# Performance work log

Hardware: AMD Instinct MI355X
Metric: run time of the kernel (lower is better)

Reference implementation:

```python
import jax, jax.numpy as jnp
import numpy as np

N_NODES = 25000
N_EDGES = 400000
D = 128            # input_dim == all gnn_latent_dim entries
N_LAYERS = 3
N_GRAPHS = 512
D_OUT = 10
BN_EPS = 1e-5


def setup_inputs() -> dict:
    key = jax.random.key(0)
    ks = jax.random.split(key, 12)
    s = 1.0 / np.sqrt(D)
    x = jax.random.normal(ks[0], (N_NODES, D), dtype=jnp.float32)
    edge_index = jax.random.randint(ks[1], (2, N_EDGES), 0, N_NODES, dtype=jnp.int64)
    batch = jnp.sort(jax.random.randint(ks[2], (N_NODES,), 0, N_GRAPHS, dtype=jnp.int64))
    W1 = jax.random.normal(ks[3], (N_LAYERS, D, D), dtype=jnp.float32) * s
    b1 = jnp.zeros((N_LAYERS, D), dtype=jnp.float32)
    gamma = jnp.ones((N_LAYERS, D), dtype=jnp.float32)
    beta = jnp.zeros((N_LAYERS, D), dtype=jnp.float32)
    run_mean = jnp.zeros((N_LAYERS, D), dtype=jnp.float32)
    run_var = jnp.ones((N_LAYERS, D), dtype=jnp.float32)
    W2 = jax.random.normal(ks[4], (N_LAYERS, D, D), dtype=jnp.float32) * s
    b2 = jnp.zeros((N_LAYERS, D), dtype=jnp.float32)
    eps = jnp.zeros((N_LAYERS,), dtype=jnp.float32)  # GIN eps, train_eps=True init 0
    Wout = jax.random.normal(ks[5], (D, D_OUT), dtype=jnp.float32) * s
    bout = jnp.zeros((D_OUT,), dtype=jnp.float32)
    return {"x": x, "edge_index": edge_index, "batch": batch,
            "W1": W1, "b1": b1, "gamma": gamma, "beta": beta,
            "run_mean": run_mean, "run_var": run_var,
            "W2": W2, "b2": b2, "eps": eps, "Wout": Wout, "bout": bout}


def reference(x, edge_index, batch, W1, b1, gamma, beta, run_mean, run_var, W2, b2, eps, Wout, bout):
    src, dst = edge_index[0], edge_index[1]
    h = x
    for i in range(N_LAYERS):
        # GIN aggregation: sum_{j in N(i)} h_j + (1 + eps) * h_i  (self loop weight 1+eps)
        agg = jax.ops.segment_sum(h[src], dst, num_segments=N_NODES)
        agg = agg + (1.0 + eps[i]) * h
        # nn: Linear -> BatchNorm1d (eval, running stats) -> ReLU -> Linear
        z = agg @ W1[i] + b1[i]
        z = (z - run_mean[i]) * jax.lax.rsqrt(run_var[i] + BN_EPS) * gamma[i] + beta[i]
        z = jax.nn.relu(z)
        z = z @ W2[i] + b2[i]
        # post-conv activation (dropout p=0 omitted)
        h = jax.nn.relu(z)
    # readout: global mean pool per graph
    ones = jnp.ones((h.shape[0],), dtype=h.dtype)
    counts = jax.ops.segment_sum(ones, batch, num_segments=N_GRAPHS)
    pooled = jax.ops.segment_sum(h, batch, num_segments=N_GRAPHS) / jnp.clip(counts, 1.0)[:, None]
    # single final Linear (fc_latent_dim=[])
    logits = pooled @ Wout + bout
    return logits
```

## Files before the change

kernel.cpp:

```cpp
#include <hip/hip_runtime.h>
#include <hip/hip_bf16.h>

#define NNODES 25000
#define NEDGES 400000
#define DIM 128
#define NGRAPHS 512
#define DOUT 10
#define NPAD 32768

typedef short bf16x8 __attribute__((ext_vector_type(8)));
typedef float f32x4 __attribute__((ext_vector_type(4)));

__device__ inline float bfu_lo(unsigned int u) {
  union { unsigned int i; float f; } v; v.i = u << 16; return v.f;
}
__device__ inline float bfu_hi(unsigned int u) {
  union { unsigned int i; float f; } v; v.i = u & 0xffff0000u; return v.f;
}
__device__ inline unsigned short f2bf(float f) {
  union { float f; unsigned int i; } v; v.f = f;
  unsigned int r = v.i + 0x7fff + ((v.i >> 16) & 1);
  return (unsigned short)(r >> 16);
}


__global__ __launch_bounds__(256) void k_deg(const int* __restrict__ dst,
                                             int* __restrict__ deg) {
  int i = blockIdx.x * 256 + threadIdx.x;
  if (i < NEDGES) atomicAdd(&deg[dst[i]], 1);
}

__global__ __launch_bounds__(1024) void k_scan(const int* __restrict__ deg,
                                               int* __restrict__ offs,
                                               int* __restrict__ cursor) {
  __shared__ int tsum[1024];
  int t = threadIdx.x;
  const int4* d4 = (const int4*)(deg + t * 32);
  int4 v[8];
#pragma unroll
  for (int j = 0; j < 8; ++j) v[j] = d4[j];
  int s = 0;
#pragma unroll
  for (int j = 0; j < 8; ++j) s += v[j].x + v[j].y + v[j].z + v[j].w;
  tsum[t] = s;
  __syncthreads();
  for (int off = 1; off < 1024; off <<= 1) {
    int u = (t >= off) ? tsum[t - off] : 0;
    __syncthreads();
    tsum[t] += u;
    __syncthreads();
  }
  int run = (t == 0) ? 0 : tsum[t - 1];
  int4* o4 = (int4*)(offs + t * 32);
  int4* c4 = (int4*)(cursor + t * 32);
#pragma unroll
  for (int j = 0; j < 8; ++j) {
    int4 w;
    w.x = run; run += v[j].x;
    w.y = run; run += v[j].y;
    w.z = run; run += v[j].z;
    w.w = run; run += v[j].w;
    o4[j] = w; c4[j] = w;
  }
}

__global__ __launch_bounds__(256) void k_scatter(const int* __restrict__ src,
                                                 const int* __restrict__ dst,
                                                 int* __restrict__ cursor,
                                                 int* __restrict__ csr) {
  int i = blockIdx.x * 256 + threadIdx.x;
  if (i < NEDGES) {
    int p = atomicAdd(&cursor[dst[i]], 1);
    csr[p] = src[i];
  }
}


__global__ __launch_bounds__(256) void k_cvt(const float* __restrict__ x,
                                             unsigned short* __restrict__ h0) {
  int i = blockIdx.x * 256 + threadIdx.x;
  if (i * 8 >= NNODES * DIM) return;
  const float4* x4 = (const float4*)x;
  float4 a = x4[i * 2], b = x4[i * 2 + 1];
  uint4 p;
  p.x = ((unsigned int)f2bf(a.y) << 16) | f2bf(a.x);
  p.y = ((unsigned int)f2bf(a.w) << 16) | f2bf(a.z);
  p.z = ((unsigned int)f2bf(b.y) << 16) | f2bf(b.x);
  p.w = ((unsigned int)f2bf(b.w) << 16) | f2bf(b.z);
  ((uint4*)h0)[i] = p;
}


__global__ __launch_bounds__(256) void k_wprep(const float* __restrict__ W1,
                                               const float* __restrict__ W2,
                                               unsigned short* __restrict__ W1T,
                                               unsigned short* __restrict__ W2T) {
  int b = blockIdx.x;
  int l = b >> 1;
  const float* in = ((b & 1) ? W2 : W1) + (size_t)l * DIM * DIM;
  unsigned short* out = ((b & 1) ? W2T : W1T) + (size_t)l * DIM * DIM;
  for (int idx = threadIdx.x; idx < DIM * DIM; idx += 256) {
    int c = idx >> 7, k = idx & 127;
    out[idx] = f2bf(in[k * DIM + c]);
  }
}


__global__ __launch_bounds__(256) void k_agg(const unsigned short* __restrict__ h,
                                             const int* __restrict__ offs,
                                             const int* __restrict__ csr,
                                             const float* __restrict__ epsp, int layer,
                                             unsigned short* __restrict__ agg) {
  int node = blockIdx.x * 8 + (threadIdx.x >> 5);
  int lane = threadIdx.x & 31;
  const uint2* h2 = (const uint2*)h;
  float eps1 = 1.0f + epsp[layer];
  int s = offs[node], e = offs[node + 1];
  uint2 hv = h2[(size_t)node * 32 + lane];
  float a0 = eps1 * bfu_lo(hv.x), a1 = eps1 * bfu_hi(hv.x);
  float a2 = eps1 * bfu_lo(hv.y), a3 = eps1 * bfu_hi(hv.y);
  float b0 = 0.f, b1 = 0.f, b2 = 0.f, b3 = 0.f;
  int j = s;
  for (; j + 3 < e; j += 4) {
    int s0 = csr[j], s1 = csr[j + 1], s2 = csr[j + 2], s3 = csr[j + 3];
    uint2 v0 = h2[(size_t)s0 * 32 + lane];
    uint2 v1 = h2[(size_t)s1 * 32 + lane];
    uint2 v2 = h2[(size_t)s2 * 32 + lane];
    uint2 v3 = h2[(size_t)s3 * 32 + lane];
    a0 += bfu_lo(v0.x); a1 += bfu_hi(v0.x); a2 += bfu_lo(v0.y); a3 += bfu_hi(v0.y);
    b0 += bfu_lo(v1.x); b1 += bfu_hi(v1.x); b2 += bfu_lo(v1.y); b3 += bfu_hi(v1.y);
    a0 += bfu_lo(v2.x); a1 += bfu_hi(v2.x); a2 += bfu_lo(v2.y); a3 += bfu_hi(v2.y);
    b0 += bfu_lo(v3.x); b1 += bfu_hi(v3.x); b2 += bfu_lo(v3.y); b3 += bfu_hi(v3.y);
  }
  for (; j < e; ++j) {
    uint2 v = h2[(size_t)csr[j] * 32 + lane];
    a0 += bfu_lo(v.x); a1 += bfu_hi(v.x); a2 += bfu_lo(v.y); a3 += bfu_hi(v.y);
  }
  a0 += b0; a1 += b1; a2 += b2; a3 += b3;
  uint2 p;
  p.x = ((unsigned int)f2bf(a1) << 16) | f2bf(a0);
  p.y = ((unsigned int)f2bf(a3) << 16) | f2bf(a2);
  ((uint2*)agg)[(size_t)node * 32 + lane] = p;
}


#define MROWS 32

__global__ __launch_bounds__(256) void k_mlp(const unsigned short* __restrict__ agg,
                                             const unsigned short* __restrict__ W1T,
                                             const unsigned short* __restrict__ W2T,
                                             const float* __restrict__ b1,
                                             const float* __restrict__ gamma,
                                             const float* __restrict__ beta,
                                             const float* __restrict__ rmean,
                                             const float* __restrict__ rvar,
                                             const float* __restrict__ b2,
                                             unsigned short* __restrict__ hout) {
  __shared__ __align__(16) char smem[MROWS * 256];
  int t = threadIdx.x;
  int lane = t & 63;
  int wv = t >> 6;
  int r0 = blockIdx.x * MROWS;
  int cl = lane & 15;
  int kg = lane >> 4;

  {
    const uint4* ag4 = (const uint4*)(agg + (size_t)r0 * DIM);
#pragma unroll
    for (int it = 0; it < 2; ++it) {
      int u = t + it * 256;
      int row = u >> 4, un = u & 15;
      uint4 v = make_uint4(0u, 0u, 0u, 0u);
      if (r0 + row < NNODES) v = ag4[u];
      *(uint4*)(smem + row * 256 + ((un * 16) ^ ((row & 7) << 4))) = v;
    }
  }

  bf16x8 b1f[2][4], b2f[2][4];
#pragma unroll
  for (int ct = 0; ct < 2; ++ct) {
    int col = wv * 32 + ct * 16 + cl;
    const char* p1 = (const char*)(W1T + (size_t)col * DIM);
    const char* p2 = (const char*)(W2T + (size_t)col * DIM);
#pragma unroll
    for (int kk = 0; kk < 4; ++kk) {
      b1f[ct][kk] = *(const bf16x8*)(p1 + kk * 64 + kg * 16);
      b2f[ct][kk] = *(const bf16x8*)(p2 + kk * 64 + kg * 16);
    }
  }
  float s1c[2], o1c[2], b2c[2];
#pragma unroll
  for (int ct = 0; ct < 2; ++ct) {
    int col = wv * 32 + ct * 16 + cl;
    float sc = gamma[col] * rsqrtf(rvar[col] + 1e-5f);
    s1c[ct] = sc;
    o1c[ct] = (b1[col] - rmean[col]) * sc + beta[col];
    b2c[ct] = b2[col];
  }
  __syncthreads();

  f32x4 zero = {0.f, 0.f, 0.f, 0.f};
  f32x4 acc[2][2] = {{zero, zero}, {zero, zero}};
#pragma unroll
  for (int kk = 0; kk < 4; ++kk) {
#pragma unroll
    for (int rt = 0; rt < 2; ++rt) {
      int row = rt * 16 + cl;
      int un = kk * 4 + kg;
      bf16x8 a = *(const bf16x8*)(smem + row * 256 + ((un * 16) ^ ((row & 7) << 4)));
      acc[rt][0] = __builtin_amdgcn_mfma_f32_16x16x32_bf16(a, b1f[0][kk], acc[rt][0], 0, 0, 0);
      acc[rt][1] = __builtin_amdgcn_mfma_f32_16x16x32_bf16(a, b1f[1][kk], acc[rt][1], 0, 0, 0);
    }
  }
  __syncthreads();

#pragma unroll
  for (int rt = 0; rt < 2; ++rt)
#pragma unroll
    for (int ct = 0; ct < 2; ++ct) {
      int col = wv * 32 + ct * 16 + cl;
#pragma unroll
      for (int j = 0; j < 4; ++j) {
        int row = rt * 16 + kg * 4 + j;
        float z = fmaxf(acc[rt][ct][j] * s1c[ct] + o1c[ct], 0.f);
        *(unsigned short*)(smem + row * 256 + ((col * 2) ^ ((row & 7) << 4))) = f2bf(z);
      }
    }
  __syncthreads();

  f32x4 acc2[2][2] = {{zero, zero}, {zero, zero}};
#pragma unroll
  for (int kk = 0; kk < 4; ++kk) {
#pragma unroll
    for (int rt = 0; rt < 2; ++rt) {
      int row = rt * 16 + cl;
      int un = kk * 4 + kg;
      bf16x8 a = *(const bf16x8*)(smem + row * 256 + ((un * 16) ^ ((row & 7) << 4)));
      acc2[rt][0] = __builtin_amdgcn_mfma_f32_16x16x32_bf16(a, b2f[0][kk], acc2[rt][0], 0, 0, 0);
      acc2[rt][1] = __builtin_amdgcn_mfma_f32_16x16x32_bf16(a, b2f[1][kk], acc2[rt][1], 0, 0, 0);
    }
  }
  __syncthreads();

#pragma unroll
  for (int rt = 0; rt < 2; ++rt)
#pragma unroll
    for (int ct = 0; ct < 2; ++ct) {
      int col = wv * 32 + ct * 16 + cl;
#pragma unroll
      for (int j = 0; j < 4; ++j) {
        int row = rt * 16 + kg * 4 + j;
        float hv = fmaxf(acc2[rt][ct][j] + b2c[ct], 0.f);
        *(unsigned short*)(smem + row * 256 + ((col * 2) ^ ((row & 7) << 4))) = f2bf(hv);
      }
    }
  __syncthreads();

  {
    uint4* ho4 = (uint4*)(hout + (size_t)r0 * DIM);
#pragma unroll
    for (int it = 0; it < 2; ++it) {
      int u = t + it * 256;
      int row = u >> 4, un = u & 15;
      if (r0 + row < NNODES) {
        uint4 v = *(const uint4*)(smem + row * 256 + ((un * 16) ^ ((row & 7) << 4)));
        ho4[u] = v;
      }
    }
  }
}


__device__ inline int lower_bound_i(const int* a, int n, int key) {
  int lo = 0, hi = n;
  while (lo < hi) {
    int m = (lo + hi) >> 1;
    if (a[m] < key) lo = m + 1; else hi = m;
  }
  return lo;
}

__global__ __launch_bounds__(256) void k_pool(const unsigned short* __restrict__ h,
                                              const int* __restrict__ batch,
                                              const float* __restrict__ Wout,
                                              const float* __restrict__ bout,
                                              float* __restrict__ out) {
  int g = blockIdx.x;
  int t = threadIdx.x;
  int cg = t & 31;
  int st = t >> 5;
  int lo = lower_bound_i(batch, NNODES, g);
  int hi = lower_bound_i(batch, NNODES, g + 1);
  const uint2* h2 = (const uint2*)h;
  float a0 = 0.f, a1 = 0.f, a2 = 0.f, a3 = 0.f;
  for (int i = lo + st; i < hi; i += 8) {
    uint2 v = h2[(size_t)i * 32 + cg];
    a0 += bfu_lo(v.x); a1 += bfu_hi(v.x); a2 += bfu_lo(v.y); a3 += bfu_hi(v.y);
  }
  __shared__ float red[8][DIM];
  __shared__ float pooled[DIM];
  red[st][cg * 4 + 0] = a0; red[st][cg * 4 + 1] = a1;
  red[st][cg * 4 + 2] = a2; red[st][cg * 4 + 3] = a3;
  __syncthreads();
  if (t < DIM) {
    float s = 0.f;
#pragma unroll
    for (int k = 0; k < 8; ++k) s += red[k][t];
    float cnt = (hi > lo) ? (float)(hi - lo) : 1.0f;
    pooled[t] = s / cnt;
  }
  __syncthreads();
  if (t < DOUT) {
    float acc = bout[t];
#pragma unroll 8
    for (int k = 0; k < DIM; ++k) acc = fmaf(pooled[k], Wout[k * DOUT + t], acc);
    out[g * DOUT + t] = acc;
  }
}


extern "C" void kernel_launch(void* const* d_in, const int* in_sizes, int n_in,
                              void* d_out, int out_size, void* d_ws, size_t ws_size,
                              hipStream_t stream) {
  const float* x     = (const float*)d_in[0];
  const int*   ei    = (const int*)d_in[1];
  const int*   batch = (const int*)d_in[2];
  const float* W1    = (const float*)d_in[3];
  const float* b1    = (const float*)d_in[4];
  const float* gamma = (const float*)d_in[5];
  const float* beta  = (const float*)d_in[6];
  const float* rmean = (const float*)d_in[7];
  const float* rvar  = (const float*)d_in[8];
  const float* W2    = (const float*)d_in[9];
  const float* b2    = (const float*)d_in[10];
  const float* eps   = (const float*)d_in[11];
  const float* Wout  = (const float*)d_in[12];
  const float* bout  = (const float*)d_in[13];
  float* out = (float*)d_out;

  const int* src = ei;
  const int* dst = ei + NEDGES;

  char* ws = (char*)d_ws;
  size_t o = 0;
  auto alloc = [&](size_t bytes) -> void* {
    o = (o + 255) & ~(size_t)255;
    void* p = ws + o;
    o += bytes;
    return p;
  };
  int* deg    = (int*)alloc(NPAD * sizeof(int));
  int* offs   = (int*)alloc((NPAD + 8) * sizeof(int));
  int* cursor = (int*)alloc(NPAD * sizeof(int));
  int* csr    = (int*)alloc(NEDGES * sizeof(int));
  unsigned short* h0  = (unsigned short*)alloc((size_t)NNODES * DIM * 2);
  unsigned short* agg = (unsigned short*)alloc((size_t)NNODES * DIM * 2);
  unsigned short* hA  = (unsigned short*)alloc((size_t)NNODES * DIM * 2);
  unsigned short* hB  = (unsigned short*)alloc((size_t)NNODES * DIM * 2);
  unsigned short* W1T = (unsigned short*)alloc(3 * DIM * DIM * 2);
  unsigned short* W2T = (unsigned short*)alloc(3 * DIM * DIM * 2);

  hipMemsetAsync(deg, 0, NPAD * sizeof(int), stream);
  k_deg<<<(NEDGES + 255) / 256, 256, 0, stream>>>(dst, deg);
  k_cvt<<<(NNODES * DIM / 8 + 255) / 256, 256, 0, stream>>>(x, h0);
  k_wprep<<<6, 256, 0, stream>>>(W1, W2, W1T, W2T);
  k_scan<<<1, 1024, 0, stream>>>(deg, offs, cursor);
  k_scatter<<<(NEDGES + 255) / 256, 256, 0, stream>>>(src, dst, cursor, csr);

  const unsigned short* hin = h0;
  unsigned short* houts[3] = {hA, hB, hA};
  for (int l = 0; l < 3; ++l) {
    k_agg<<<NNODES / 8, 256, 0, stream>>>(hin, offs, csr, eps, l, agg);
    k_mlp<<<(NNODES + MROWS - 1) / MROWS, 256, 0, stream>>>(
        agg, W1T + (size_t)l * DIM * DIM, W2T + (size_t)l * DIM * DIM,
        b1 + l * DIM, gamma + l * DIM, beta + l * DIM, rmean + l * DIM,
        rvar + l * DIM, b2 + l * DIM, houts[l]);
    hin = houts[l];
  }
  k_pool<<<NGRAPHS, 256, 0, stream>>>(hin, batch, Wout, bout, out);
}
```

Before: 255.8 us.

## Fuse GIN neighbor aggregation into the MLP kernel via shared memory

Removes the separate aggregation kernel. Each wavefront of the MLP kernel now gathers and sums neighbor rows for 8 nodes, one 32-bit bf16 pair per lane, and writes the result straight into the swizzled shared-memory tile that feeds the MFMA matmuls. This drops the agg buffer's global write and read and one launch per layer. The cost is less gather parallelism per block (8 rows per wave, processed one after another), and the gather latency now sits in front of the matmul stage in the same block, which may lower latency hiding and occupancy.

```diff
diff --git a/kernel.cpp b/kernel.cpp
--- a/kernel.cpp
+++ b/kernel.cpp
@@ -106,47 +106,12 @@
 }
 
 
-__global__ __launch_bounds__(256) void k_agg(const unsigned short* __restrict__ h,
+#define MROWS 32
+
+__global__ __launch_bounds__(256) void k_mlp(const unsigned short* __restrict__ h,
                                              const int* __restrict__ offs,
                                              const int* __restrict__ csr,
                                              const float* __restrict__ epsp, int layer,
-                                             unsigned short* __restrict__ agg) {
-  int node = blockIdx.x * 8 + (threadIdx.x >> 5);
-  int lane = threadIdx.x & 31;
-  const uint2* h2 = (const uint2*)h;
-  float eps1 = 1.0f + epsp[layer];
-  int s = offs[node], e = offs[node + 1];
-  uint2 hv = h2[(size_t)node * 32 + lane];
-  float a0 = eps1 * bfu_lo(hv.x), a1 = eps1 * bfu_hi(hv.x);
-  float a2 = eps1 * bfu_lo(hv.y), a3 = eps1 * bfu_hi(hv.y);
-  float b0 = 0.f, b1 = 0.f, b2 = 0.f, b3 = 0.f;
-  int j = s;
-  for (; j + 3 < e; j += 4) {
-    int s0 = csr[j], s1 = csr[j + 1], s2 = csr[j + 2], s3 = csr[j + 3];
-    uint2 v0 = h2[(size_t)s0 * 32 + lane];
-    uint2 v1 = h2[(size_t)s1 * 32 + lane];
-    uint2 v2 = h2[(size_t)s2 * 32 + lane];
-    uint2 v3 = h2[(size_t)s3 * 32 + lane];
-    a0 += bfu_lo(v0.x); a1 += bfu_hi(v0.x); a2 += bfu_lo(v0.y); a3 += bfu_hi(v0.y);
-    b0 += bfu_lo(v1.x); b1 += bfu_hi(v1.x); b2 += bfu_lo(v1.y); b3 += bfu_hi(v1.y);
-    a0 += bfu_lo(v2.x); a1 += bfu_hi(v2.x); a2 += bfu_lo(v2.y); a3 += bfu_hi(v2.y);
-    b0 += bfu_lo(v3.x); b1 += bfu_hi(v3.x); b2 += bfu_lo(v3.y); b3 += bfu_hi(v3.y);
-  }
-  for (; j < e; ++j) {
-    uint2 v = h2[(size_t)csr[j] * 32 + lane];
-    a0 += bfu_lo(v.x); a1 += bfu_hi(v.x); a2 += bfu_lo(v.y); a3 += bfu_hi(v.y);
-  }
-  a0 += b0; a1 += b1; a2 += b2; a3 += b3;
-  uint2 p;
-  p.x = ((unsigned int)f2bf(a1) << 16) | f2bf(a0);
-  p.y = ((unsigned int)f2bf(a3) << 16) | f2bf(a2);
-  ((uint2*)agg)[(size_t)node * 32 + lane] = p;
-}
-
-
-#define MROWS 32
-
-__global__ __launch_bounds__(256) void k_mlp(const unsigned short* __restrict__ agg,
                                              const unsigned short* __restrict__ W1T,
                                              const unsigned short* __restrict__ W2T,
                                              const float* __restrict__ b1,
@@ -163,17 +128,50 @@
   int r0 = blockIdx.x * MROWS;
   int cl = lane & 15;
   int kg = lane >> 4;
-
-  {
-    const uint4* ag4 = (const uint4*)(agg + (size_t)r0 * DIM);
-#pragma unroll
-    for (int it = 0; it < 2; ++it) {
-      int u = t + it * 256;
-      int row = u >> 4, un = u & 15;
-      uint4 v = make_uint4(0u, 0u, 0u, 0u);
-      if (r0 + row < NNODES) v = ag4[u];
-      *(uint4*)(smem + row * 256 + ((un * 16) ^ ((row & 7) << 4))) = v;
-    }
+  float eps1 = 1.0f + epsp[layer];
+
+  const unsigned int* hw = (const unsigned int*)h;
+#pragma unroll
+  for (int rr = 0; rr < 8; ++rr) {
+    int row = wv * 8 + rr;
+    int node = r0 + row;
+    unsigned int pk = 0u;
+    if (node < NNODES) {
+      int s = __builtin_amdgcn_readfirstlane(offs[node]);
+      int e = __builtin_amdgcn_readfirstlane(offs[node + 1]);
+      unsigned int hv = hw[(size_t)node * 64 + lane];
+      float a0 = eps1 * bfu_lo(hv), a1 = eps1 * bfu_hi(hv);
+      float p0 = 0.f, p1 = 0.f, q0 = 0.f, q1 = 0.f, u0 = 0.f, u1 = 0.f;
+      int j = s;
+      for (; j + 7 < e; j += 8) {
+        int s0 = csr[j + 0], s1 = csr[j + 1], s2 = csr[j + 2], s3 = csr[j + 3];
+        int s4 = csr[j + 4], s5 = csr[j + 5], s6 = csr[j + 6], s7 = csr[j + 7];
+        unsigned int v0 = hw[(size_t)s0 * 64 + lane];
+        unsigned int v1 = hw[(size_t)s1 * 64 + lane];
+        unsigned int v2 = hw[(size_t)s2 * 64 + lane];
+        unsigned int v3 = hw[(size_t)s3 * 64 + lane];
+        unsigned int v4 = hw[(size_t)s4 * 64 + lane];
+        unsigned int v5 = hw[(size_t)s5 * 64 + lane];
+        unsigned int v6 = hw[(size_t)s6 * 64 + lane];
+        unsigned int v7 = hw[(size_t)s7 * 64 + lane];
+        a0 += bfu_lo(v0); a1 += bfu_hi(v0);
+        p0 += bfu_lo(v1); p1 += bfu_hi(v1);
+        q0 += bfu_lo(v2); q1 += bfu_hi(v2);
+        u0 += bfu_lo(v3); u1 += bfu_hi(v3);
+        a0 += bfu_lo(v4); a1 += bfu_hi(v4);
+        p0 += bfu_lo(v5); p1 += bfu_hi(v5);
+        q0 += bfu_lo(v6); q1 += bfu_hi(v6);
+        u0 += bfu_lo(v7); u1 += bfu_hi(v7);
+      }
+      for (; j < e; ++j) {
+        unsigned int v = hw[(size_t)csr[j] * 64 + lane];
+        a0 += bfu_lo(v); a1 += bfu_hi(v);
+      }
+      a0 += p0 + q0 + u0;
+      a1 += p1 + q1 + u1;
+      pk = ((unsigned int)f2bf(a1) << 16) | f2bf(a0);
+    }
+    *(unsigned int*)(smem + row * 256 + ((lane * 4) ^ ((row & 7) << 4))) = pk;
   }
 
   bf16x8 b1f[2][4], b2f[2][4];
@@ -354,7 +352,6 @@
   int* cursor = (int*)alloc(NPAD * sizeof(int));
   int* csr    = (int*)alloc(NEDGES * sizeof(int));
   unsigned short* h0  = (unsigned short*)alloc((size_t)NNODES * DIM * 2);
-  unsigned short* agg = (unsigned short*)alloc((size_t)NNODES * DIM * 2);
   unsigned short* hA  = (unsigned short*)alloc((size_t)NNODES * DIM * 2);
   unsigned short* hB  = (unsigned short*)alloc((size_t)NNODES * DIM * 2);
   unsigned short* W1T = (unsigned short*)alloc(3 * DIM * DIM * 2);
@@ -370,9 +367,9 @@
   const unsigned short* hin = h0;
   unsigned short* houts[3] = {hA, hB, hA};
   for (int l = 0; l < 3; ++l) {
-    k_agg<<<NNODES / 8, 256, 0, stream>>>(hin, offs, csr, eps, l, agg);
     k_mlp<<<(NNODES + MROWS - 1) / MROWS, 256, 0, stream>>>(
-        agg, W1T + (size_t)l * DIM * DIM, W2T + (size_t)l * DIM * DIM,
+        hin, offs, csr, eps, l,
+        W1T + (size_t)l * DIM * DIM, W2T + (size_t)l * DIM * DIM,
         b1 + l * DIM, gamma + l * DIM, beta + l * DIM, rmean + l * DIM,
         rvar + l * DIM, b2 + l * DIM, houts[l]);
     hin = houts[l];
```

New measurement: 270.6 us. 5.8% more time.

## Fuse prep kernels and split aggregation feature dimension across two block halves

Applied to the files above, without the earlier changes.

Merges the degree count, input bf16 conversion and weight transpose kernels into one launch using block-index ranges, cutting two launches. The gather aggregation now splits each node's 128 features into two halves handled by separate blocks, with each lane loading 4 bytes instead of 8. The neighbor loop is unrolled to 8 with five independent accumulator pairs to keep more loads in flight. This doubles the grid and the CSR index and offset reads, and each gathered row access becomes 128 bytes rather than 256.

```diff
diff --git a/kernel.cpp b/kernel.cpp
--- a/kernel.cpp
+++ b/kernel.cpp
@@ -7,6 +7,7 @@
 #define NGRAPHS 512
 #define DOUT 10
 #define NPAD 32768
+#define AGG_NB (NNODES / 8)
 
 typedef short bf16x8 __attribute__((ext_vector_type(8)));
 typedef float f32x4 __attribute__((ext_vector_type(4)));
@@ -24,11 +25,42 @@
 }
 
 
-__global__ __launch_bounds__(256) void k_deg(const int* __restrict__ dst,
-                                             int* __restrict__ deg) {
-  int i = blockIdx.x * 256 + threadIdx.x;
-  if (i < NEDGES) atomicAdd(&deg[dst[i]], 1);
-}
+__global__ __launch_bounds__(256) void k_prep(const int* __restrict__ dst,
+                                              int* __restrict__ deg,
+                                              const float* __restrict__ x,
+                                              unsigned short* __restrict__ h0,
+                                              const float* __restrict__ W1,
+                                              const float* __restrict__ W2,
+                                              unsigned short* __restrict__ W1T,
+                                              unsigned short* __restrict__ W2T) {
+  int b = blockIdx.x;
+  if (b < 1563) {
+    int i = b * 256 + threadIdx.x;
+    if (i < NEDGES) atomicAdd(&deg[dst[i]], 1);
+  } else if (b < 3126) {
+    int i = (b - 1563) * 256 + threadIdx.x;
+    if (i * 8 < NNODES * DIM) {
+      const float4* x4 = (const float4*)x;
+      float4 a = x4[i * 2], c = x4[i * 2 + 1];
+      uint4 p;
+      p.x = ((unsigned int)f2bf(a.y) << 16) | f2bf(a.x);
+      p.y = ((unsigned int)f2bf(a.w) << 16) | f2bf(a.z);
+      p.z = ((unsigned int)f2bf(c.y) << 16) | f2bf(c.x);
+      p.w = ((unsigned int)f2bf(c.w) << 16) | f2bf(c.z);
+      ((uint4*)h0)[i] = p;
+    }
+  } else {
+    int wb = b - 3126;
+    int l = wb >> 1;
+    const float* in = ((wb & 1) ? W2 : W1) + (size_t)l * DIM * DIM;
+    unsigned short* out = ((wb & 1) ? W2T : W1T) + (size_t)l * DIM * DIM;
+    for (int idx = threadIdx.x; idx < DIM * DIM; idx += 256) {
+      int c = idx >> 7, k = idx & 127;
+      out[idx] = f2bf(in[k * DIM + c]);
+    }
+  }
+}
+
 
 __global__ __launch_bounds__(1024) void k_scan(const int* __restrict__ deg,
                                                int* __restrict__ offs,
@@ -76,71 +108,60 @@
 }
 
 
-__global__ __launch_bounds__(256) void k_cvt(const float* __restrict__ x,
-                                             unsigned short* __restrict__ h0) {
-  int i = blockIdx.x * 256 + threadIdx.x;
-  if (i * 8 >= NNODES * DIM) return;
-  const float4* x4 = (const float4*)x;
-  float4 a = x4[i * 2], b = x4[i * 2 + 1];
-  uint4 p;
-  p.x = ((unsigned int)f2bf(a.y) << 16) | f2bf(a.x);
-  p.y = ((unsigned int)f2bf(a.w) << 16) | f2bf(a.z);
-  p.z = ((unsigned int)f2bf(b.y) << 16) | f2bf(b.x);
-  p.w = ((unsigned int)f2bf(b.w) << 16) | f2bf(b.z);
-  ((uint4*)h0)[i] = p;
-}
-
-
-__global__ __launch_bounds__(256) void k_wprep(const float* __restrict__ W1,
-                                               const float* __restrict__ W2,
-                                               unsigned short* __restrict__ W1T,
-                                               unsigned short* __restrict__ W2T) {
-  int b = blockIdx.x;
-  int l = b >> 1;
-  const float* in = ((b & 1) ? W2 : W1) + (size_t)l * DIM * DIM;
-  unsigned short* out = ((b & 1) ? W2T : W1T) + (size_t)l * DIM * DIM;
-  for (int idx = threadIdx.x; idx < DIM * DIM; idx += 256) {
-    int c = idx >> 7, k = idx & 127;
-    out[idx] = f2bf(in[k * DIM + c]);
-  }
-}
-
-
 __global__ __launch_bounds__(256) void k_agg(const unsigned short* __restrict__ h,
                                              const int* __restrict__ offs,
                                              const int* __restrict__ csr,
                                              const float* __restrict__ epsp, int layer,
                                              unsigned short* __restrict__ agg) {
-  int node = blockIdx.x * 8 + (threadIdx.x >> 5);
+  int blk = blockIdx.x;
+  int half = (blk >= AGG_NB) ? 1 : 0;
+  int nb = blk - half * AGG_NB;
+  int node = nb * 8 + (threadIdx.x >> 5);
   int lane = threadIdx.x & 31;
-  const uint2* h2 = (const uint2*)h;
+  int base = half * 32 + lane;
+  const unsigned int* hw = (const unsigned int*)h;
   float eps1 = 1.0f + epsp[layer];
   int s = offs[node], e = offs[node + 1];
-  uint2 hv = h2[(size_t)node * 32 + lane];
-  float a0 = eps1 * bfu_lo(hv.x), a1 = eps1 * bfu_hi(hv.x);
-  float a2 = eps1 * bfu_lo(hv.y), a3 = eps1 * bfu_hi(hv.y);
-  float b0 = 0.f, b1 = 0.f, b2 = 0.f, b3 = 0.f;
+  unsigned int hv = hw[(size_t)node * 64 + base];
+  float a0 = eps1 * bfu_lo(hv), a1 = eps1 * bfu_hi(hv);
+  float b0 = 0.f, b1 = 0.f, c0 = 0.f, c1 = 0.f;
+  float d0 = 0.f, d1 = 0.f, g0 = 0.f, g1 = 0.f;
   int j = s;
-  for (; j + 3 < e; j += 4) {
-    int s0 = csr[j], s1 = csr[j + 1], s2 = csr[j + 2], s3 = csr[j + 3];
-    uint2 v0 = h2[(size_t)s0 * 32 + lane];
-    uint2 v1 = h2[(size_t)s1 * 32 + lane];
-    uint2 v2 = h2[(size_t)s2 * 32 + lane];
-    uint2 v3 = h2[(size_t)s3 * 32 + lane];
-    a0 += bfu_lo(v0.x); a1 += bfu_hi(v0.x); a2 += bfu_lo(v0.y); a3 += bfu_hi(v0.y);
-    b0 += bfu_lo(v1.x); b1 += bfu_hi(v1.x); b2 += bfu_lo(v1.y); b3 += bfu_hi(v1.y);
-    a0 += bfu_lo(v2.x); a1 += bfu_hi(v2.x); a2 += bfu_lo(v2.y); a3 += bfu_hi(v2.y);
-    b0 += bfu_lo(v3.x); b1 += bfu_hi(v3.x); b2 += bfu_lo(v3.y); b3 += bfu_hi(v3.y);
-  }
-  for (; j < e; ++j) {
-    uint2 v = h2[(size_t)csr[j] * 32 + lane];
-    a0 += bfu_lo(v.x); a1 += bfu_hi(v.x); a2 += bfu_lo(v.y); a3 += bfu_hi(v.y);
-  }
-  a0 += b0; a1 += b1; a2 += b2; a3 += b3;
-  uint2 p;
-  p.x = ((unsigned int)f2bf(a1) << 16) | f2bf(a0);
-  p.y = ((unsigned int)f2bf(a3) << 16) | f2bf(a2);
-  ((uint2*)agg)[(size_t)node * 32 + lane] = p;
+  for (; j + 7 < e; j += 8) {
+    int s0 = csr[j + 0], s1 = csr[j + 1], s2 = csr[j + 2], s3 = csr[j + 3];
+    int s4 = csr[j + 4], s5 = csr[j + 5], s6 = csr[j + 6], s7 = csr[j + 7];
+    unsigned int v0 = hw[(size_t)s0 * 64 + base];
+    unsigned int v1 = hw[(size_t)s1 * 64 + base];
+    unsigned int v2 = hw[(size_t)s2 * 64 + base];
+    unsigned int v3 = hw[(size_t)s3 * 64 + base];
+    unsigned int v4 = hw[(size_t)s4 * 64 + base];
+    unsigned int v5 = hw[(size_t)s5 * 64 + base];
+    unsigned int v6 = hw[(size_t)s6 * 64 + base];
+    unsigned int v7 = hw[(size_t)s7 * 64 + base];
+    a0 += bfu_lo(v0); a1 += bfu_hi(v0);
+    b0 += bfu_lo(v1); b1 += bfu_hi(v1);
+    c0 += bfu_lo(v2); c1 += bfu_hi(v2);
+    d0 += bfu_lo(v3); d1 += bfu_hi(v3);
+    g0 += bfu_lo(v4); g1 += bfu_hi(v4);
+    a0 += bfu_lo(v5); a1 += bfu_hi(v5);
+    b0 += bfu_lo(v6); b1 += bfu_hi(v6);
+    c0 += bfu_lo(v7); c1 += bfu_hi(v7);
+  }
+  for (; j + 1 < e; j += 2) {
+    int s0 = csr[j], s1 = csr[j + 1];
+    unsigned int v0 = hw[(size_t)s0 * 64 + base];
+    unsigned int v1 = hw[(size_t)s1 * 64 + base];
+    a0 += bfu_lo(v0); a1 += bfu_hi(v0);
+    b0 += bfu_lo(v1); b1 += bfu_hi(v1);
+  }
+  if (j < e) {
+    unsigned int v = hw[(size_t)csr[j] * 64 + base];
+    a0 += bfu_lo(v); a1 += bfu_hi(v);
+  }
+  a0 += b0 + c0 + d0 + g0;
+  a1 += b1 + c1 + d1 + g1;
+  ((unsigned int*)agg)[(size_t)node * 64 + base] =
+      ((unsigned int)f2bf(a1) << 16) | f2bf(a0);
 }
 
 
@@ -361,16 +382,14 @@
   unsigned short* W2T = (unsigned short*)alloc(3 * DIM * DIM * 2);
 
   hipMemsetAsync(deg, 0, NPAD * sizeof(int), stream);
-  k_deg<<<(NEDGES + 255) / 256, 256, 0, stream>>>(dst, deg);
-  k_cvt<<<(NNODES * DIM / 8 + 255) / 256, 256, 0, stream>>>(x, h0);
-  k_wprep<<<6, 256, 0, stream>>>(W1, W2, W1T, W2T);
+  k_prep<<<3132, 256, 0, stream>>>(dst, deg, x, h0, W1, W2, W1T, W2T);
   k_scan<<<1, 1024, 0, stream>>>(deg, offs, cursor);
   k_scatter<<<(NEDGES + 255) / 256, 256, 0, stream>>>(src, dst, cursor, csr);
 
   const unsigned short* hin = h0;
   unsigned short* houts[3] = {hA, hB, hA};
   for (int l = 0; l < 3; ++l) {
-    k_agg<<<NNODES / 8, 256, 0, stream>>>(hin, offs, csr, eps, l, agg);
+    k_agg<<<AGG_NB * 2, 256, 0, stream>>>(hin, offs, csr, eps, l, agg);
     k_mlp<<<(NNODES + MROWS - 1) / MROWS, 256, 0, stream>>>(
         agg, W1T + (size_t)l * DIM * DIM, W2T + (size_t)l * DIM * DIM,
         b1 + l * DIM, gamma + l * DIM, beta + l * DIM, rmean + l * DIM,
```

Result: no change. 256.8 us (+0.4%).
